# Optimization experiments

Measured on AMD Instinct MI355X. Metric: run time of the kernel, lower is better.

The kernel has to match this reference:

```python
import jax, jax.numpy as jnp
import numpy as np

N = 50000   # num nodes (agents)
E = 1200000 # num directed edges
F_NODE = 5
F_EDGE = 2
H = 64      # hidden_dim


def _mlp2(x, W1, b1, W2, b2):
    return jax.nn.relu(x @ W1 + b1) @ W2 + b2


def setup_inputs() -> dict:
    key = jax.random.key(0)
    ks = jax.random.split(key, 16)
    def glorot(k, shape):
        fan_in = shape[0]
        return jax.random.normal(k, shape, dtype=jnp.float32) / jnp.sqrt(jnp.float32(fan_in))
    x = jax.random.normal(ks[0], (N, F_NODE), dtype=jnp.float32)
    edge_attr = jax.random.normal(ks[1], (E, F_EDGE), dtype=jnp.float32)
    edge_index = jax.random.randint(ks[2], (2, E), 0, N, dtype=jnp.int32)
    return {
        "x": x,
        "edge_attr": edge_attr,
        "edge_index": edge_index,
        # node encoder: Linear(5,H) -> ReLU -> Linear(H,H)
        "Wn1": glorot(ks[3], (F_NODE, H)), "bn1": jnp.zeros((H,), jnp.float32),
        "Wn2": glorot(ks[4], (H, H)),      "bn2": jnp.zeros((H,), jnp.float32),
        # edge encoder: Linear(2,H)
        "We": glorot(ks[5], (F_EDGE, H)),  "be": jnp.zeros((H,), jnp.float32),
        # message net: Linear(3H,H) -> ReLU -> Linear(H,H)
        "Wm1": glorot(ks[6], (3 * H, H)),  "bm1": jnp.zeros((H,), jnp.float32),
        "Wm2": glorot(ks[7], (H, H)),      "bm2": jnp.zeros((H,), jnp.float32),
        # update net: Linear(2H,H) -> ReLU -> Linear(H,H)
        "Wu1": glorot(ks[8], (2 * H, H)),  "bu1": jnp.zeros((H,), jnp.float32),
        "Wu2": glorot(ks[9], (H, H)),      "bu2": jnp.zeros((H,), jnp.float32),
    }


def reference(x, edge_attr, edge_index,
              Wn1, bn1, Wn2, bn2,
              We, be,
              Wm1, bm1, Wm2, bm2,
              Wu1, bu1, Wu2, bu2):
    n = x.shape[0]
    # encoders
    h = _mlp2(x, Wn1, bn1, Wn2, bn2)          # [N, H]
    e = edge_attr @ We + be                    # [E, H]
    # PyG flow source_to_target: x_j = x[src=row 0], x_i = x[dst=row 1]
    src = edge_index[0]
    dst = edge_index[1]
    m_in = jnp.concatenate([h[dst], h[src], e], axis=-1)  # [E, 3H]
    m = _mlp2(m_in, Wm1, bm1, Wm2, bm2)        # [E, H]
    # mean aggregation at target nodes
    msum = jax.ops.segment_sum(m, dst, num_segments=n)                # [N, H]
    cnt = jax.ops.segment_sum(jnp.ones((m.shape[0],), m.dtype), dst, num_segments=n)
    agg = msum / jnp.maximum(cnt, 1.0)[:, None]
    # update
    out = _mlp2(jnp.concatenate([h, agg], axis=-1), Wu1, bu1, Wu2, bu2)
    return out
```

## Files before the change

### kernel.cpp

```cpp
#include <hip/hip_runtime.h>
#include <hip/hip_bf16.h>

#define NN 50000
#define NE 1200000
#define H 64
#define NBUCK 196
#define CHUNK 4096
#define NCHUNK ((NE + CHUNK - 1) / CHUNK)

using bf16x8 = __attribute__((ext_vector_type(8))) short;
using f32x4  = __attribute__((ext_vector_type(4))) float;

static __device__ __forceinline__ unsigned short f2bf(float f) {
    __hip_bfloat16 h = __float2bfloat16(f);
    return *reinterpret_cast<unsigned short*>(&h);
}
static __device__ __forceinline__ float bf2f(unsigned short u) {
    return __uint_as_float((unsigned)u << 16);
}

__global__ __launch_bounds__(256) void k0_prep(
    const float* __restrict__ We, const float* __restrict__ be,
    const float* __restrict__ Wm1, const float* __restrict__ bm1,
    const float* __restrict__ Wm2, const float* __restrict__ bm2,
    const float* __restrict__ Wu1,
    float* __restrict__ We2, float* __restrict__ bp,
    float* __restrict__ Wma, float* __restrict__ bma)
{
    const int tid = threadIdx.x;
    const int j = tid & (H - 1);
    const int q = tid >> 6;
    if (q == 0) {
        float s0 = 0.f, s1 = 0.f, sb = 0.f;
        for (int k = 0; k < H; ++k) {
            const float w = Wm1[(2 * H + k) * H + j];
            s0 = fmaf(We[k], w, s0);
            s1 = fmaf(We[H + k], w, s1);
            sb = fmaf(be[k], w, sb);
        }
        We2[j]     = s0;
        We2[H + j] = s1;
        bp[j]      = sb + bm1[j];
        float sm = 0.f;
        for (int l = 0; l < H; ++l)
            sm = fmaf(bm2[l], Wu1[(H + l) * H + j], sm);
        bma[j] = sm;
    }
    for (int k = q * (H / 4); k < (q + 1) * (H / 4); ++k) {
        float s = 0.f;
        for (int l = 0; l < H; ++l)
            s = fmaf(Wm2[k * H + l], Wu1[(H + l) * H + j], s);
        Wma[k * H + j] = s;
    }
}

__global__ __launch_bounds__(256) void k1_mfma(
    const float* __restrict__ x,
    const float* __restrict__ Wn1, const float* __restrict__ bn1,
    const float* __restrict__ Wn2, const float* __restrict__ bn2,
    const float* __restrict__ Wm1, const float* __restrict__ Wu1,
    unsigned short* __restrict__ Ab, unsigned short* __restrict__ Bb,
    unsigned short* __restrict__ HUb)
{
    __shared__ unsigned short hbuf[4][16 * 64];
    __shared__ bf16x8 wfrag[4][4][2][64];

    const int tid = threadIdx.x;
    const int w   = tid >> 6;
    const int l   = tid & 63;
    const int l15 = l & 15;
    const int lb  = l >> 4;

    const float* Wmats[4] = { Wn2, Wm1, Wm1 + H * H, Wu1 };
    const float* Wsrc = Wmats[w];
#pragma unroll
    for (int t = 0; t < 4; ++t)
#pragma unroll
        for (int kh = 0; kh < 2; ++kh) {
            bf16x8 f;
#pragma unroll
            for (int j = 0; j < 8; ++j) {
                const int k = kh * 32 + lb * 8 + j;
                f[j] = (short)f2bf(Wsrc[k * H + 16 * t + l15]);
            }
            wfrag[w][t][kh][l] = f;
        }

    bf16x8 b1frag[4];
    float bn1t[4], bn2t[4];
#pragma unroll
    for (int t = 0; t < 4; ++t) {
        bn1t[t] = bn1[16 * t + l15];
        bn2t[t] = bn2[16 * t + l15];
#pragma unroll
        for (int j = 0; j < 8; ++j) {
            float v = (lb == 0 && j < 5) ? Wn1[j * H + 16 * t + l15] : 0.f;
            b1frag[t][j] = (short)f2bf(v);
        }
    }
    __syncthreads();

    const int g = blockIdx.x * 4 + w;
    if (g * 16 >= NN) return;
    const int n0 = g * 16;
    const f32x4 z4 = {0.f, 0.f, 0.f, 0.f};

    bf16x8 xf = {0, 0, 0, 0, 0, 0, 0, 0};
    if (lb == 0) {
        const float* xr = x + (size_t)(n0 + l15) * 5;
#pragma unroll
        for (int j = 0; j < 5; ++j) xf[j] = (short)f2bf(xr[j]);
    }
    f32x4 acc1[4];
#pragma unroll
    for (int t = 0; t < 4; ++t)
        acc1[t] = __builtin_amdgcn_mfma_f32_16x16x32_bf16(xf, b1frag[t], z4, 0, 0, 0);
#pragma unroll
    for (int t = 0; t < 4; ++t)
#pragma unroll
        for (int q = 0; q < 4; ++q) {
            const int m = lb * 4 + q;
            const int idx = (m * 64 + 16 * t + l15) ^ ((m & 7) << 3);
            hbuf[w][idx] = f2bf(fmaxf(acc1[t][q] + bn1t[t], 0.f));
        }
    __builtin_amdgcn_wave_barrier();

    auto rdA = [&](int kh) {
        const int idx = (l15 * 64 + kh * 32 + lb * 8) ^ ((l15 & 7) << 3);
        return *reinterpret_cast<const bf16x8*>(&hbuf[w][idx]);
    };

    {
        bf16x8 a0 = rdA(0), a1 = rdA(1);
        __builtin_amdgcn_wave_barrier();
        f32x4 acc[4];
#pragma unroll
        for (int t = 0; t < 4; ++t) {
            acc[t] = __builtin_amdgcn_mfma_f32_16x16x32_bf16(a0, wfrag[0][t][0][l], z4, 0, 0, 0);
            acc[t] = __builtin_amdgcn_mfma_f32_16x16x32_bf16(a1, wfrag[0][t][1][l], acc[t], 0, 0, 0);
        }
#pragma unroll
        for (int t = 0; t < 4; ++t)
#pragma unroll
            for (int q = 0; q < 4; ++q) {
                const int m = lb * 4 + q;
                const int idx = (m * 64 + 16 * t + l15) ^ ((m & 7) << 3);
                hbuf[w][idx] = f2bf(acc[t][q] + bn2t[t]);
            }
        __builtin_amdgcn_wave_barrier();
    }

    bf16x8 h0 = rdA(0), h1v = rdA(1);
#pragma unroll
    for (int t = 0; t < 4; ++t) {
        f32x4 acc = __builtin_amdgcn_mfma_f32_16x16x32_bf16(h0, wfrag[1][t][0][l], z4, 0, 0, 0);
        acc = __builtin_amdgcn_mfma_f32_16x16x32_bf16(h1v, wfrag[1][t][1][l], acc, 0, 0, 0);
#pragma unroll
        for (int q = 0; q < 4; ++q)
            Ab[(size_t)(n0 + lb * 4 + q) * H + 16 * t + l15] = f2bf(acc[q]);
    }
#pragma unroll
    for (int t = 0; t < 4; ++t) {
        f32x4 acc = __builtin_amdgcn_mfma_f32_16x16x32_bf16(h0, wfrag[2][t][0][l], z4, 0, 0, 0);
        acc = __builtin_amdgcn_mfma_f32_16x16x32_bf16(h1v, wfrag[2][t][1][l], acc, 0, 0, 0);
#pragma unroll
        for (int q = 0; q < 4; ++q)
            Bb[(size_t)(n0 + lb * 4 + q) * H + 16 * t + l15] = f2bf(acc[q]);
    }
#pragma unroll
    for (int t = 0; t < 4; ++t) {
        f32x4 acc = __builtin_amdgcn_mfma_f32_16x16x32_bf16(h0, wfrag[3][t][0][l], z4, 0, 0, 0);
        acc = __builtin_amdgcn_mfma_f32_16x16x32_bf16(h1v, wfrag[3][t][1][l], acc, 0, 0, 0);
#pragma unroll
        for (int q = 0; q < 4; ++q)
            HUb[(size_t)(n0 + lb * 4 + q) * H + 16 * t + l15] = f2bf(acc[q]);
    }
}

__global__ __launch_bounds__(256) void k2h0(
    const int* __restrict__ eidx, int* __restrict__ gbcnt)
{
    __shared__ int hl[NBUCK];
    const int tid = threadIdx.x;
    for (int i = tid; i < NBUCK; i += 256) hl[i] = 0;
    __syncthreads();
    const int stride = gridDim.x * 256;
    for (int e = blockIdx.x * 256 + tid; e < NE; e += stride)
        atomicAdd(&hl[eidx[NE + e] >> 8], 1);
    __syncthreads();
    for (int i = tid; i < NBUCK; i += 256)
        if (hl[i]) atomicAdd(&gbcnt[i], hl[i]);
}

__global__ __launch_bounds__(256) void k2h1(
    const int* __restrict__ gbcnt, int* __restrict__ bbase, int* __restrict__ gcur)
{
    __shared__ int wsum[4];
    const int tid = threadIdx.x, lane = tid & 63, wv = tid >> 6;
    const int v = (tid < NBUCK) ? gbcnt[tid] : 0;
    int s = v;
#pragma unroll
    for (int d = 1; d < 64; d <<= 1) {
        int t = __shfl_up(s, (unsigned)d, 64);
        if (lane >= d) s += t;
    }
    if (lane == 63) wsum[wv] = s;
    __syncthreads();
    int wb = 0;
#pragma unroll
    for (int k = 0; k < 4; ++k) wb += (k < wv) ? wsum[k] : 0;
    const int excl = wb + s - v;
    if (tid < NBUCK) {
        bbase[tid] = excl;
        gcur[tid]  = excl;
        if (tid == NBUCK - 1) bbase[NBUCK] = excl + v;
    }
}

__global__ __launch_bounds__(256) void k2s_sort(
    const int* __restrict__ eidx, const float* __restrict__ ea,
    int* __restrict__ gcur, uint2* __restrict__ rec)
{
    __shared__ int hcnt[256], delta[256], c2[256];
    __shared__ int wsum[4];
    __shared__ uint2 srt[CHUNK];
    const int tid = threadIdx.x, lane = tid & 63, wv = tid >> 6;
    const int cbase = blockIdx.x * CHUNK;
    const int nck = (NE - cbase < CHUNK) ? (NE - cbase) : CHUNK;

    hcnt[tid] = 0;
    __syncthreads();

    unsigned rx[16], ry[16];
#pragma unroll
    for (int k = 0; k < 16; ++k) {
        const int i = k * 256 + tid;
        if (i < nck) {
            const int e = cbase + i;
            const int dst = eidx[NE + e];
            const int src = eidx[e];
            const float2 q = ((const float2*)ea)[e];
            rx[k] = (unsigned)src | ((unsigned)(dst & 255) << 16)
                  | ((unsigned)(dst >> 8) << 24);
            ry[k] = (unsigned)f2bf(q.x) | ((unsigned)f2bf(q.y) << 16);
            atomicAdd(&hcnt[dst >> 8], 1);
        } else rx[k] = 0xFFFFFFFFu;
    }
    __syncthreads();

    const int v = hcnt[tid];
    int s = v;
#pragma unroll
    for (int d = 1; d < 64; d <<= 1) {
        int t = __shfl_up(s, (unsigned)d, 64);
        if (lane >= d) s += t;
    }
    if (lane == 63) wsum[wv] = s;
    __syncthreads();
    int wb = 0;
#pragma unroll
    for (int k = 0; k < 4; ++k) wb += (k < wv) ? wsum[k] : 0;
    const int excl = wb + s - v;
    c2[tid] = excl;
    if (tid < NBUCK) {
        const int base = v ? atomicAdd(&gcur[tid], v) : 0;
        delta[tid] = base - excl;
    }
    __syncthreads();

#pragma unroll
    for (int k = 0; k < 16; ++k) {
        if (rx[k] != 0xFFFFFFFFu) {
            const int b = rx[k] >> 24;
            const int slot = atomicAdd(&c2[b], 1);
            srt[slot] = (uint2){rx[k], ry[k]};
        }
    }
    __syncthreads();

    for (int i = tid; i < nck; i += 256) {
        const uint2 rr = srt[i];
        rec[i + delta[rr.x >> 24]] = rr;
    }
}

__global__ __launch_bounds__(256) void k2d_csr(
    const int* __restrict__ bbase, const uint2* __restrict__ rec,
    int* __restrict__ off, uint2* __restrict__ rec2)
{
    __shared__ int hl[256], c2[256];
    __shared__ int wsum[4];
    const int tid = threadIdx.x, lane = tid & 63, wv = tid >> 6;
    const int b = blockIdx.x;
    const int r0 = bbase[b], r1 = bbase[b + 1];
    const int nr = r1 - r0;

    hl[tid] = 0;
    __syncthreads();
    for (int i = tid; i < nr; i += 256)
        atomicAdd(&hl[(rec[r0 + i].x >> 16) & 255], 1);
    __syncthreads();

    const int v = hl[tid];
    int s = v;
#pragma unroll
    for (int d = 1; d < 64; d <<= 1) {
        int t = __shfl_up(s, (unsigned)d, 64);
        if (lane >= d) s += t;
    }
    if (lane == 63) wsum[wv] = s;
    __syncthreads();
    int wb = 0;
#pragma unroll
    for (int k = 0; k < 4; ++k) wb += (k < wv) ? wsum[k] : 0;
    const int excl = wb + s - v;
    c2[tid] = r0 + excl;
    const int n = b * 256 + tid;
    if (n < NN) off[n] = r0 + excl;
    if (b == NBUCK - 1 && tid == 0) off[NN] = NE;
    __syncthreads();

    for (int i = tid; i < nr; i += 256) {
        const uint2 rr = rec[r0 + i];
        const int ln = (rr.x >> 16) & 255;
        const int pos = atomicAdd(&c2[ln], 1);
        rec2[pos] = (uint2){rr.x & 0xFFFFu, rr.y};
    }
}

__global__ __launch_bounds__(256, 8) void k3r_agg(
    const int* __restrict__ off, const uint2* __restrict__ rec2,
    const unsigned short* __restrict__ Ab, const unsigned short* __restrict__ Bb,
    const float* __restrict__ We2, const float* __restrict__ bp,
    unsigned short* __restrict__ Rb)
{
    const int j = threadIdx.x & 63;
    const int wid = (blockIdx.x * 256 + threadIdx.x) >> 6;
    const int nw = (gridDim.x * 256) >> 6;
    const float w0 = We2[j], w1 = We2[H + j], bpj = bp[j];

    for (int n = wid; n < NN; n += nw) {
        const int e0 = __builtin_amdgcn_readfirstlane(off[n]);
        const int e1 = __builtin_amdgcn_readfirstlane(off[n + 1]);
        const float a = bf2f(Ab[(size_t)n * H + j]) + bpj;
        float rsum = 0.f;

        auto proc = [&](unsigned rx, unsigned ry) {
            const float bb = bf2f(Bb[(size_t)(rx & 0xFFFFu) * H + j]);
            float z = a + bb;
            z = fmaf(__uint_as_float(ry << 16), w0, z);
            z = fmaf(__uint_as_float(ry & 0xFFFF0000u), w1, z);
            rsum += fmaxf(z, 0.f);
        };

        int e = e0;
        if ((e & 1) && e < e1) {
            const uint2 r = rec2[e];
            proc(r.x, r.y);
            ++e;
        }
        for (; e + 8 <= e1; e += 8) {
            const uint4 p0 = *(const uint4*)(rec2 + e);
            const uint4 p1 = *(const uint4*)(rec2 + e + 2);
            const uint4 p2 = *(const uint4*)(rec2 + e + 4);
            const uint4 p3 = *(const uint4*)(rec2 + e + 6);
            proc(p0.x, p0.y); proc(p0.z, p0.w);
            proc(p1.x, p1.y); proc(p1.z, p1.w);
            proc(p2.x, p2.y); proc(p2.z, p2.w);
            proc(p3.x, p3.y); proc(p3.z, p3.w);
        }
        for (; e + 2 <= e1; e += 2) {
            const uint4 p0 = *(const uint4*)(rec2 + e);
            proc(p0.x, p0.y); proc(p0.z, p0.w);
        }
        if (e < e1) {
            const uint2 r = rec2[e];
            proc(r.x, r.y);
        }
        Rb[(size_t)n * H + j] = f2bf(rsum);
    }
}

__global__ __launch_bounds__(256) void k4_mfma(
    const int* __restrict__ off,
    const unsigned short* __restrict__ Rb, const unsigned short* __restrict__ HUb,
    const float* __restrict__ Wma, const float* __restrict__ bma,
    const float* __restrict__ bu1,
    const float* __restrict__ Wu2, const float* __restrict__ bu2,
    float* __restrict__ out)
{
    __shared__ unsigned short hbuf[4][16 * 64];
    __shared__ bf16x8 wfrag[2][4][2][64];

    const int tid = threadIdx.x;
    const int w   = tid >> 6;
    const int l   = tid & 63;
    const int l15 = l & 15;
    const int lb  = l >> 4;

    if (w < 2) {
        const float* Wsrc = (w == 0) ? Wma : Wu2;
#pragma unroll
        for (int t = 0; t < 4; ++t)
#pragma unroll
            for (int kh = 0; kh < 2; ++kh) {
                bf16x8 f;
#pragma unroll
                for (int j = 0; j < 8; ++j) {
                    const int k = kh * 32 + lb * 8 + j;
                    f[j] = (short)f2bf(Wsrc[k * H + 16 * t + l15]);
                }
                wfrag[w][t][kh][l] = f;
            }
    }
    __syncthreads();

    const int g = blockIdx.x * 4 + w;
    if (g * 16 >= NN) return;
    const int n0 = g * 16;
    const f32x4 z4 = {0.f, 0.f, 0.f, 0.f};

    const bf16x8 r0 = *(const bf16x8*)(Rb + (size_t)(n0 + l15) * H + lb * 8);
    const bf16x8 r1 = *(const bf16x8*)(Rb + (size_t)(n0 + l15) * H + 32 + lb * 8);

    const float cntv = (float)(off[n0 + l15 + 1] - off[n0 + l15]);

    float bmat[4], bu1t[4], bu2t[4];
#pragma unroll
    for (int t = 0; t < 4; ++t) {
        bmat[t] = bma[16 * t + l15];
        bu1t[t] = bu1[16 * t + l15];
        bu2t[t] = bu2[16 * t + l15];
    }

#pragma unroll
    for (int t = 0; t < 4; ++t) {
        f32x4 acc = __builtin_amdgcn_mfma_f32_16x16x32_bf16(r0, wfrag[0][t][0][l], z4, 0, 0, 0);
        acc = __builtin_amdgcn_mfma_f32_16x16x32_bf16(r1, wfrag[0][t][1][l], acc, 0, 0, 0);
#pragma unroll
        for (int q = 0; q < 4; ++q) {
            const int row = lb * 4 + q;
            const float c  = __shfl(cntv, row, 64);
            const float cc = fmaxf(c, 1.0f);
            const float hu = bf2f(HUb[(size_t)(n0 + row) * H + 16 * t + l15]);
            float z = hu + fmaf(c, bmat[t], acc[q]) / cc + bu1t[t];
            z = fmaxf(z, 0.f);
            const int idx = (row * 64 + 16 * t + l15) ^ ((row & 7) << 3);
            hbuf[w][idx] = f2bf(z);
        }
    }
    __builtin_amdgcn_wave_barrier();

    const int ia0 = (l15 * 64 + 0  + lb * 8) ^ ((l15 & 7) << 3);
    const int ia1 = (l15 * 64 + 32 + lb * 8) ^ ((l15 & 7) << 3);
    const bf16x8 a0 = *reinterpret_cast<const bf16x8*>(&hbuf[w][ia0]);
    const bf16x8 a1 = *reinterpret_cast<const bf16x8*>(&hbuf[w][ia1]);

#pragma unroll
    for (int t = 0; t < 4; ++t) {
        f32x4 acc = __builtin_amdgcn_mfma_f32_16x16x32_bf16(a0, wfrag[1][t][0][l], z4, 0, 0, 0);
        acc = __builtin_amdgcn_mfma_f32_16x16x32_bf16(a1, wfrag[1][t][1][l], acc, 0, 0, 0);
#pragma unroll
        for (int q = 0; q < 4; ++q)
            out[(size_t)(n0 + lb * 4 + q) * H + 16 * t + l15] = acc[q] + bu2t[t];
    }
}

extern "C" void kernel_launch(void* const* d_in, const int* in_sizes, int n_in,
                              void* d_out, int out_size, void* d_ws, size_t ws_size,
                              hipStream_t stream) {
    (void)in_sizes; (void)n_in; (void)out_size; (void)ws_size;
    const float* x    = (const float*)d_in[0];
    const float* eatt = (const float*)d_in[1];
    const int*   eidx = (const int*)d_in[2];
    const float* Wn1  = (const float*)d_in[3];
    const float* bn1  = (const float*)d_in[4];
    const float* Wn2  = (const float*)d_in[5];
    const float* bn2  = (const float*)d_in[6];
    const float* We   = (const float*)d_in[7];
    const float* be   = (const float*)d_in[8];
    const float* Wm1  = (const float*)d_in[9];
    const float* bm1  = (const float*)d_in[10];
    const float* Wm2  = (const float*)d_in[11];
    const float* bm2  = (const float*)d_in[12];
    const float* Wu1  = (const float*)d_in[13];
    const float* bu1  = (const float*)d_in[14];
    const float* Wu2  = (const float*)d_in[15];
    const float* bu2  = (const float*)d_in[16];
    float* out = (float*)d_out;

    char* wsb = (char*)d_ws;
    unsigned short* Ab  = (unsigned short*)wsb;
    unsigned short* Bb  = Ab + (size_t)NN * H;
    unsigned short* HUb = Bb + (size_t)NN * H;
    unsigned short* Rb  = HUb + (size_t)NN * H;
    uint2* rec  = (uint2*)(Rb + (size_t)NN * H);
    uint2* rec2 = rec + NE;
    int*   off  = (int*)(rec2 + NE);
    int*   bbase= off + NN + 1;
    int*   gbcnt= bbase + NBUCK + 1;
    int*   gcur = gbcnt + NBUCK;
    float* We2  = (float*)(gcur + NBUCK);
    float* bp   = We2 + 2 * H;
    float* Wma  = bp + H;
    float* bma  = Wma + H * H;

    hipMemsetAsync(gbcnt, 0, NBUCK * sizeof(int), stream);

    k0_prep<<<1, 256, 0, stream>>>(We, be, Wm1, bm1, Wm2, bm2, Wu1,
                                   We2, bp, Wma, bma);
    k1_mfma<<<(NN / 16 + 3) / 4, 256, 0, stream>>>(x, Wn1, bn1, Wn2, bn2,
                                                   Wm1, Wu1, Ab, Bb, HUb);
    k2h0<<<1024, 256, 0, stream>>>(eidx, gbcnt);
    k2h1<<<1, 256, 0, stream>>>(gbcnt, bbase, gcur);
    k2s_sort<<<NCHUNK, 256, 0, stream>>>(eidx, eatt, gcur, rec);
    k2d_csr<<<NBUCK, 256, 0, stream>>>(bbase, rec, off, rec2);
    k3r_agg<<<2048, 256, 0, stream>>>(off, rec2, Ab, Bb, We2, bp, Rb);
    k4_mfma<<<(NN / 16 + 3) / 4, 256, 0, stream>>>(off, Rb, HUb, Wma, bma,
                                                   bu1, Wu2, bu2, out);
}
```

Measured before the change: 250.3 us.

## Merge node encoder with histogram, scan with prep, stage CSR scatter in LDS

```diff
diff --git a/kernel.cpp b/kernel.cpp
--- a/kernel.cpp
+++ b/kernel.cpp
@@ -7,6 +7,9 @@
 #define NBUCK 196
 #define CHUNK 4096
 #define NCHUNK ((NE + CHUNK - 1) / CHUNK)
+#define K1B 782
+#define HISTB 256
+#define MAXB 7000
 
 using bf16x8 = __attribute__((ext_vector_type(8))) short;
 using f32x4  = __attribute__((ext_vector_type(4))) float;
@@ -19,7 +22,147 @@
     return __uint_as_float((unsigned)u << 16);
 }
 
-__global__ __launch_bounds__(256) void k0_prep(
+__global__ __launch_bounds__(256) void kA_node_hist(
+    const float* __restrict__ x,
+    const float* __restrict__ Wn1, const float* __restrict__ bn1,
+    const float* __restrict__ Wn2, const float* __restrict__ bn2,
+    const float* __restrict__ Wm1, const float* __restrict__ Wu1,
+    const int* __restrict__ eidx,
+    unsigned short* __restrict__ Ab, unsigned short* __restrict__ Bb,
+    unsigned short* __restrict__ HUb, int* __restrict__ gbcnt)
+{
+    __shared__ unsigned short hbuf[4][16 * 64];
+    __shared__ bf16x8 wfrag[4][4][2][64];
+
+    const int tid = threadIdx.x;
+
+    if (blockIdx.x >= K1B) {
+        int* hl = (int*)&hbuf[0][0];
+        for (int i = tid; i < NBUCK; i += 256) hl[i] = 0;
+        __syncthreads();
+        const int hb = blockIdx.x - K1B;
+        const int stride = HISTB * 256;
+        for (int e = hb * 256 + tid; e < NE; e += stride)
+            atomicAdd(&hl[eidx[NE + e] >> 8], 1);
+        __syncthreads();
+        for (int i = tid; i < NBUCK; i += 256)
+            if (hl[i]) atomicAdd(&gbcnt[i], hl[i]);
+        return;
+    }
+
+    const int w   = tid >> 6;
+    const int l   = tid & 63;
+    const int l15 = l & 15;
+    const int lb  = l >> 4;
+
+    const float* Wmats[4] = { Wn2, Wm1, Wm1 + H * H, Wu1 };
+    const float* Wsrc = Wmats[w];
+#pragma unroll
+    for (int t = 0; t < 4; ++t)
+#pragma unroll
+        for (int kh = 0; kh < 2; ++kh) {
+            bf16x8 f;
+#pragma unroll
+            for (int j = 0; j < 8; ++j) {
+                const int k = kh * 32 + lb * 8 + j;
+                f[j] = (short)f2bf(Wsrc[k * H + 16 * t + l15]);
+            }
+            wfrag[w][t][kh][l] = f;
+        }
+
+    bf16x8 b1frag[4];
+    float bn1t[4], bn2t[4];
+#pragma unroll
+    for (int t = 0; t < 4; ++t) {
+        bn1t[t] = bn1[16 * t + l15];
+        bn2t[t] = bn2[16 * t + l15];
+#pragma unroll
+        for (int j = 0; j < 8; ++j) {
+            float v = (lb == 0 && j < 5) ? Wn1[j * H + 16 * t + l15] : 0.f;
+            b1frag[t][j] = (short)f2bf(v);
+        }
+    }
+    __syncthreads();
+
+    const int g = blockIdx.x * 4 + w;
+    if (g * 16 >= NN) return;
+    const int n0 = g * 16;
+    const f32x4 z4 = {0.f, 0.f, 0.f, 0.f};
+
+    bf16x8 xf = {0, 0, 0, 0, 0, 0, 0, 0};
+    if (lb == 0) {
+        const float* xr = x + (size_t)(n0 + l15) * 5;
+#pragma unroll
+        for (int j = 0; j < 5; ++j) xf[j] = (short)f2bf(xr[j]);
+    }
+    f32x4 acc1[4];
+#pragma unroll
+    for (int t = 0; t < 4; ++t)
+        acc1[t] = __builtin_amdgcn_mfma_f32_16x16x32_bf16(xf, b1frag[t], z4, 0, 0, 0);
+#pragma unroll
+    for (int t = 0; t < 4; ++t)
+#pragma unroll
+        for (int q = 0; q < 4; ++q) {
+            const int m = lb * 4 + q;
+            const int idx = (m * 64 + 16 * t + l15) ^ ((m & 7) << 3);
+            hbuf[w][idx] = f2bf(fmaxf(acc1[t][q] + bn1t[t], 0.f));
+        }
+    __builtin_amdgcn_wave_barrier();
+
+    auto rdA = [&](int kh) {
+        const int idx = (l15 * 64 + kh * 32 + lb * 8) ^ ((l15 & 7) << 3);
+        return *reinterpret_cast<const bf16x8*>(&hbuf[w][idx]);
+    };
+
+    {
+        bf16x8 a0 = rdA(0), a1 = rdA(1);
+        __builtin_amdgcn_wave_barrier();
+        f32x4 acc[4];
+#pragma unroll
+        for (int t = 0; t < 4; ++t) {
+            acc[t] = __builtin_amdgcn_mfma_f32_16x16x32_bf16(a0, wfrag[0][t][0][l], z4, 0, 0, 0);
+            acc[t] = __builtin_amdgcn_mfma_f32_16x16x32_bf16(a1, wfrag[0][t][1][l], acc[t], 0, 0, 0);
+        }
+#pragma unroll
+        for (int t = 0; t < 4; ++t)
+#pragma unroll
+            for (int q = 0; q < 4; ++q) {
+                const int m = lb * 4 + q;
+                const int idx = (m * 64 + 16 * t + l15) ^ ((m & 7) << 3);
+                hbuf[w][idx] = f2bf(acc[t][q] + bn2t[t]);
+            }
+        __builtin_amdgcn_wave_barrier();
+    }
+
+    bf16x8 h0 = rdA(0), h1v = rdA(1);
+#pragma unroll
+    for (int t = 0; t < 4; ++t) {
+        f32x4 acc = __builtin_amdgcn_mfma_f32_16x16x32_bf16(h0, wfrag[1][t][0][l], z4, 0, 0, 0);
+        acc = __builtin_amdgcn_mfma_f32_16x16x32_bf16(h1v, wfrag[1][t][1][l], acc, 0, 0, 0);
+#pragma unroll
+        for (int q = 0; q < 4; ++q)
+            Ab[(size_t)(n0 + lb * 4 + q) * H + 16 * t + l15] = f2bf(acc[q]);
+    }
+#pragma unroll
+    for (int t = 0; t < 4; ++t) {
+        f32x4 acc = __builtin_amdgcn_mfma_f32_16x16x32_bf16(h0, wfrag[2][t][0][l], z4, 0, 0, 0);
+        acc = __builtin_amdgcn_mfma_f32_16x16x32_bf16(h1v, wfrag[2][t][1][l], acc, 0, 0, 0);
+#pragma unroll
+        for (int q = 0; q < 4; ++q)
+            Bb[(size_t)(n0 + lb * 4 + q) * H + 16 * t + l15] = f2bf(acc[q]);
+    }
+#pragma unroll
+    for (int t = 0; t < 4; ++t) {
+        f32x4 acc = __builtin_amdgcn_mfma_f32_16x16x32_bf16(h0, wfrag[3][t][0][l], z4, 0, 0, 0);
+        acc = __builtin_amdgcn_mfma_f32_16x16x32_bf16(h1v, wfrag[3][t][1][l], acc, 0, 0, 0);
+#pragma unroll
+        for (int q = 0; q < 4; ++q)
+            HUb[(size_t)(n0 + lb * 4 + q) * H + 16 * t + l15] = f2bf(acc[q]);
+    }
+}
+
+__global__ __launch_bounds__(256) void kB_scan_prep(
+    const int* __restrict__ gbcnt, int* __restrict__ bbase, int* __restrict__ gcur,
     const float* __restrict__ We, const float* __restrict__ be,
     const float* __restrict__ Wm1, const float* __restrict__ bm1,
     const float* __restrict__ Wm2, const float* __restrict__ bm2,
@@ -27,7 +170,28 @@
     float* __restrict__ We2, float* __restrict__ bp,
     float* __restrict__ Wma, float* __restrict__ bma)
 {
-    const int tid = threadIdx.x;
+    __shared__ int wsum[4];
+    const int tid = threadIdx.x, lane = tid & 63, wv = tid >> 6;
+
+    const int v = (tid < NBUCK) ? gbcnt[tid] : 0;
+    int s = v;
+#pragma unroll
+    for (int d = 1; d < 64; d <<= 1) {
+        int t = __shfl_up(s, (unsigned)d, 64);
+        if (lane >= d) s += t;
+    }
+    if (lane == 63) wsum[wv] = s;
+    __syncthreads();
+    int wb = 0;
+#pragma unroll
+    for (int k = 0; k < 4; ++k) wb += (k < wv) ? wsum[k] : 0;
+    const int excl = wb + s - v;
+    if (tid < NBUCK) {
+        bbase[tid] = excl;
+        gcur[tid]  = excl;
+        if (tid == NBUCK - 1) bbase[NBUCK] = excl + v;
+    }
+
     const int j = tid & (H - 1);
     const int q = tid >> 6;
     if (q == 0) {
@@ -47,173 +211,10 @@
         bma[j] = sm;
     }
     for (int k = q * (H / 4); k < (q + 1) * (H / 4); ++k) {
-        float s = 0.f;
+        float s2 = 0.f;
         for (int l = 0; l < H; ++l)
-            s = fmaf(Wm2[k * H + l], Wu1[(H + l) * H + j], s);
-        Wma[k * H + j] = s;
-    }
-}
-
-__global__ __launch_bounds__(256) void k1_mfma(
-    const float* __restrict__ x,
-    const float* __restrict__ Wn1, const float* __restrict__ bn1,
-    const float* __restrict__ Wn2, const float* __restrict__ bn2,
-    const float* __restrict__ Wm1, const float* __restrict__ Wu1,
-    unsigned short* __restrict__ Ab, unsigned short* __restrict__ Bb,
-    unsigned short* __restrict__ HUb)
-{
-    __shared__ unsigned short hbuf[4][16 * 64];
-    __shared__ bf16x8 wfrag[4][4][2][64];
-
-    const int tid = threadIdx.x;
-    const int w   = tid >> 6;
-    const int l   = tid & 63;
-    const int l15 = l & 15;
-    const int lb  = l >> 4;
-
-    const float* Wmats[4] = { Wn2, Wm1, Wm1 + H * H, Wu1 };
-    const float* Wsrc = Wmats[w];
-#pragma unroll
-    for (int t = 0; t < 4; ++t)
-#pragma unroll
-        for (int kh = 0; kh < 2; ++kh) {
-            bf16x8 f;
-#pragma unroll
-            for (int j = 0; j < 8; ++j) {
-                const int k = kh * 32 + lb * 8 + j;
-                f[j] = (short)f2bf(Wsrc[k * H + 16 * t + l15]);
-            }
-            wfrag[w][t][kh][l] = f;
-        }
-
-    bf16x8 b1frag[4];
-    float bn1t[4], bn2t[4];
-#pragma unroll
-    for (int t = 0; t < 4; ++t) {
-        bn1t[t] = bn1[16 * t + l15];
-        bn2t[t] = bn2[16 * t + l15];
-#pragma unroll
-        for (int j = 0; j < 8; ++j) {
-            float v = (lb == 0 && j < 5) ? Wn1[j * H + 16 * t + l15] : 0.f;
-            b1frag[t][j] = (short)f2bf(v);
-        }
-    }
-    __syncthreads();
-
-    const int g = blockIdx.x * 4 + w;
-    if (g * 16 >= NN) return;
-    const int n0 = g * 16;
-    const f32x4 z4 = {0.f, 0.f, 0.f, 0.f};
-
-    bf16x8 xf = {0, 0, 0, 0, 0, 0, 0, 0};
-    if (lb == 0) {
-        const float* xr = x + (size_t)(n0 + l15) * 5;
-#pragma unroll
-        for (int j = 0; j < 5; ++j) xf[j] = (short)f2bf(xr[j]);
-    }
-    f32x4 acc1[4];
-#pragma unroll
-    for (int t = 0; t < 4; ++t)
-        acc1[t] = __builtin_amdgcn_mfma_f32_16x16x32_bf16(xf, b1frag[t], z4, 0, 0, 0);
-#pragma unroll
-    for (int t = 0; t < 4; ++t)
-#pragma unroll
-        for (int q = 0; q < 4; ++q) {
-            const int m = lb * 4 + q;
-            const int idx = (m * 64 + 16 * t + l15) ^ ((m & 7) << 3);
-            hbuf[w][idx] = f2bf(fmaxf(acc1[t][q] + bn1t[t], 0.f));
-        }
-    __builtin_amdgcn_wave_barrier();
-
-    auto rdA = [&](int kh) {
-        const int idx = (l15 * 64 + kh * 32 + lb * 8) ^ ((l15 & 7) << 3);
-        return *reinterpret_cast<const bf16x8*>(&hbuf[w][idx]);
-    };
-
-    {
-        bf16x8 a0 = rdA(0), a1 = rdA(1);
-        __builtin_amdgcn_wave_barrier();
-        f32x4 acc[4];
-#pragma unroll
-        for (int t = 0; t < 4; ++t) {
-            acc[t] = __builtin_amdgcn_mfma_f32_16x16x32_bf16(a0, wfrag[0][t][0][l], z4, 0, 0, 0);
-            acc[t] = __builtin_amdgcn_mfma_f32_16x16x32_bf16(a1, wfrag[0][t][1][l], acc[t], 0, 0, 0);
-        }
-#pragma unroll
-        for (int t = 0; t < 4; ++t)
-#pragma unroll
-            for (int q = 0; q < 4; ++q) {
-                const int m = lb * 4 + q;
-                const int idx = (m * 64 + 16 * t + l15) ^ ((m & 7) << 3);
-                hbuf[w][idx] = f2bf(acc[t][q] + bn2t[t]);
-            }
-        __builtin_amdgcn_wave_barrier();
-    }
-
-    bf16x8 h0 = rdA(0), h1v = rdA(1);
-#pragma unroll
-    for (int t = 0; t < 4; ++t) {
-        f32x4 acc = __builtin_amdgcn_mfma_f32_16x16x32_bf16(h0, wfrag[1][t][0][l], z4, 0, 0, 0);
-        acc = __builtin_amdgcn_mfma_f32_16x16x32_bf16(h1v, wfrag[1][t][1][l], acc, 0, 0, 0);
-#pragma unroll
-        for (int q = 0; q < 4; ++q)
-            Ab[(size_t)(n0 + lb * 4 + q) * H + 16 * t + l15] = f2bf(acc[q]);
-    }
-#pragma unroll
-    for (int t = 0; t < 4; ++t) {
-        f32x4 acc = __builtin_amdgcn_mfma_f32_16x16x32_bf16(h0, wfrag[2][t][0][l], z4, 0, 0, 0);
-        acc = __builtin_amdgcn_mfma_f32_16x16x32_bf16(h1v, wfrag[2][t][1][l], acc, 0, 0, 0);
-#pragma unroll
-        for (int q = 0; q < 4; ++q)
-            Bb[(size_t)(n0 + lb * 4 + q) * H + 16 * t + l15] = f2bf(acc[q]);
-    }
-#pragma unroll
-    for (int t = 0; t < 4; ++t) {
-        f32x4 acc = __builtin_amdgcn_mfma_f32_16x16x32_bf16(h0, wfrag[3][t][0][l], z4, 0, 0, 0);
-        acc = __builtin_amdgcn_mfma_f32_16x16x32_bf16(h1v, wfrag[3][t][1][l], acc, 0, 0, 0);
-#pragma unroll
-        for (int q = 0; q < 4; ++q)
-            HUb[(size_t)(n0 + lb * 4 + q) * H + 16 * t + l15] = f2bf(acc[q]);
-    }
-}
-
-__global__ __launch_bounds__(256) void k2h0(
-    const int* __restrict__ eidx, int* __restrict__ gbcnt)
-{
-    __shared__ int hl[NBUCK];
-    const int tid = threadIdx.x;
-    for (int i = tid; i < NBUCK; i += 256) hl[i] = 0;
-    __syncthreads();
-    const int stride = gridDim.x * 256;
-    for (int e = blockIdx.x * 256 + tid; e < NE; e += stride)
-        atomicAdd(&hl[eidx[NE + e] >> 8], 1);
-    __syncthreads();
-    for (int i = tid; i < NBUCK; i += 256)
-        if (hl[i]) atomicAdd(&gbcnt[i], hl[i]);
-}
-
-__global__ __launch_bounds__(256) void k2h1(
-    const int* __restrict__ gbcnt, int* __restrict__ bbase, int* __restrict__ gcur)
-{
-    __shared__ int wsum[4];
-    const int tid = threadIdx.x, lane = tid & 63, wv = tid >> 6;
-    const int v = (tid < NBUCK) ? gbcnt[tid] : 0;
-    int s = v;
-#pragma unroll
-    for (int d = 1; d < 64; d <<= 1) {
-        int t = __shfl_up(s, (unsigned)d, 64);
-        if (lane >= d) s += t;
-    }
-    if (lane == 63) wsum[wv] = s;
-    __syncthreads();
-    int wb = 0;
-#pragma unroll
-    for (int k = 0; k < 4; ++k) wb += (k < wv) ? wsum[k] : 0;
-    const int excl = wb + s - v;
-    if (tid < NBUCK) {
-        bbase[tid] = excl;
-        gcur[tid]  = excl;
-        if (tid == NBUCK - 1) bbase[NBUCK] = excl + v;
+            s2 = fmaf(Wm2[k * H + l], Wu1[(H + l) * H + j], s2);
+        Wma[k * H + j] = s2;
     }
 }
 
@@ -288,8 +289,10 @@
     const int* __restrict__ bbase, const uint2* __restrict__ rec,
     int* __restrict__ off, uint2* __restrict__ rec2)
 {
-    __shared__ int hl[256], c2[256];
+    __shared__ int hl[256];
+    __shared__ int cur[256];
     __shared__ int wsum[4];
+    __shared__ uint2 srt[MAXB];
     const int tid = threadIdx.x, lane = tid & 63, wv = tid >> 6;
     const int b = blockIdx.x;
     const int r0 = bbase[b], r1 = bbase[b + 1];
@@ -314,17 +317,29 @@
 #pragma unroll
     for (int k = 0; k < 4; ++k) wb += (k < wv) ? wsum[k] : 0;
     const int excl = wb + s - v;
-    c2[tid] = r0 + excl;
+    cur[tid] = excl;
     const int n = b * 256 + tid;
     if (n < NN) off[n] = r0 + excl;
     if (b == NBUCK - 1 && tid == 0) off[NN] = NE;
     __syncthreads();
 
-    for (int i = tid; i < nr; i += 256) {
-        const uint2 rr = rec[r0 + i];
-        const int ln = (rr.x >> 16) & 255;
-        const int pos = atomicAdd(&c2[ln], 1);
-        rec2[pos] = (uint2){rr.x & 0xFFFFu, rr.y};
+    if (nr <= MAXB) {
+        for (int i = tid; i < nr; i += 256) {
+            const uint2 rr = rec[r0 + i];
+            const int ln = (rr.x >> 16) & 255;
+            const int slot = atomicAdd(&cur[ln], 1);
+            srt[slot] = (uint2){rr.x & 0xFFFFu, rr.y};
+        }
+        __syncthreads();
+        for (int i = tid; i < nr; i += 256)
+            rec2[r0 + i] = srt[i];
+    } else {
+        for (int i = tid; i < nr; i += 256) {
+            const uint2 rr = rec[r0 + i];
+            const int ln = (rr.x >> 16) & 255;
+            const int slot = atomicAdd(&cur[ln], 1);
+            rec2[r0 + slot] = (uint2){rr.x & 0xFFFFu, rr.y};
+        }
     }
 }
 
@@ -507,12 +522,12 @@
 
     hipMemsetAsync(gbcnt, 0, NBUCK * sizeof(int), stream);
 
-    k0_prep<<<1, 256, 0, stream>>>(We, be, Wm1, bm1, Wm2, bm2, Wu1,
-                                   We2, bp, Wma, bma);
-    k1_mfma<<<(NN / 16 + 3) / 4, 256, 0, stream>>>(x, Wn1, bn1, Wn2, bn2,
-                                                   Wm1, Wu1, Ab, Bb, HUb);
-    k2h0<<<1024, 256, 0, stream>>>(eidx, gbcnt);
-    k2h1<<<1, 256, 0, stream>>>(gbcnt, bbase, gcur);
+    kA_node_hist<<<K1B + HISTB, 256, 0, stream>>>(x, Wn1, bn1, Wn2, bn2,
+                                                  Wm1, Wu1, eidx,
+                                                  Ab, Bb, HUb, gbcnt);
+    kB_scan_prep<<<1, 256, 0, stream>>>(gbcnt, bbase, gcur,
+                                        We, be, Wm1, bm1, Wm2, bm2, Wu1,
+                                        We2, bp, Wma, bma);
     k2s_sort<<<NCHUNK, 256, 0, stream>>>(eidx, eatt, gcur, rec);
     k2d_csr<<<NBUCK, 256, 0, stream>>>(bbase, rec, off, rec2);
     k3r_agg<<<2048, 256, 0, stream>>>(off, rec2, Ab, Bb, We2, bp, Rb);
```

Result: faster. 220.7 us, median of 2 (-11.8%).
